# Kernel tuning notes

Hardware: AMD Instinct MI355X
Metric: run time of the kernel (lower is better)

Reference implementation:

```python
import jax, jax.numpy as jnp
import numpy as np

B, C = 32768, 1000

def setup_inputs() -> dict:
    key = jax.random.key(0)
    k1, k2 = jax.random.split(key)
    pred = jax.random.normal(k1, (B, C), dtype=jnp.float32)
    target = jax.random.randint(k2, (B,), 0, C, dtype=jnp.int64)
    return {"pred": pred, "target": target}

def reference(pred, target):
    b, c = pred.shape
    # histogram of labels: replaces the per-class Python loop
    class_freq = jnp.zeros((c,), dtype=pred.dtype).at[target].add(1.0)
    # exp(pred) * freq, then log-normalize over classes (balanced softmax)
    scaled = jnp.exp(pred) * class_freq  # [B, C]
    log_norm = jnp.log(jnp.sum(scaled, axis=1, keepdims=True))  # [B, 1]
    logits = jnp.log(scaled) - log_norm  # [B, C]
    # one-hot multiply + sum == gather logit at target class
    picked = jnp.take_along_axis(logits, target[:, None], axis=1)  # [B, 1]
    return -jnp.sum(picked) / b
```

## Files before the change

### kernel.cpp

```cpp
#include <hip/hip_runtime.h>

#define B_ROWS 32768
#define C_COLS 1000
#define NF4 250
#define MAIN_BLOCKS 2048
#define WAVES_TOTAL (MAIN_BLOCKS * 4)
#define HIST_BLOCKS 16
#define BINS_PER_BLOCK 64

__global__ __launch_bounds__(256) void bsl_hist(const int* __restrict__ target,
                                                float* __restrict__ freq) {
    __shared__ unsigned int lh[1024];
    const int tid = threadIdx.x;
    #pragma unroll
    for (int i = tid; i < 1024; i += 256) lh[i] = 0u;
    __syncthreads();
    const int4* t4 = reinterpret_cast<const int4*>(target);
    #pragma unroll 8
    for (int k = 0; k < 32; ++k) {
        int4 v = t4[tid + k * 256];
        atomicAdd(&lh[v.x], 1u);
        atomicAdd(&lh[v.y], 1u);
        atomicAdd(&lh[v.z], 1u);
        atomicAdd(&lh[v.w], 1u);
    }
    __syncthreads();
    if (tid < BINS_PER_BLOCK) {
        const int bin = blockIdx.x * BINS_PER_BLOCK + tid;
        freq[bin] = (float)lh[bin];
    }
}

__global__ __launch_bounds__(256) void bsl_main(const float* __restrict__ pred,
                                                const int* __restrict__ target,
                                                const float* __restrict__ freq,
                                                float* __restrict__ partials) {
    __shared__ float sfreq[C_COLS];
    __shared__ float swave[4];
    const int tid = threadIdx.x;
    const int lane = tid & 63;
    const int wib = tid >> 6;

    for (int i = tid; i < C_COLS; i += 256) sfreq[i] = freq[i];
    __syncthreads();
    const float4* sf4 = reinterpret_cast<const float4*>(sfreq);

    const int gwid = blockIdx.x * 4 + wib;
    float local = 0.0f;

    for (int row = gwid; row < B_ROWS; row += WAVES_TOTAL) {
        const int t = target[row];
        const float4* prow = reinterpret_cast<const float4*>(pred + (size_t)row * C_COLS);
        const int t4i = t >> 2, tm = t & 3;
        float partial = 0.0f, pt = 0.0f;
        #pragma unroll
        for (int k = 0; k < 4; ++k) {
            const int j = k * 64 + lane;
            if (j < NF4) {
                const float4 v = prow[j];
                const float4 f = sf4[j];
                partial += __expf(v.x) * f.x + __expf(v.y) * f.y
                         + __expf(v.z) * f.z + __expf(v.w) * f.w;
                if (j == t4i)
                    pt = (tm & 1) ? ((tm & 2) ? v.w : v.y)
                                  : ((tm & 2) ? v.z : v.x);
            }
        }
        #pragma unroll
        for (int off = 32; off > 0; off >>= 1)
            partial += __shfl_xor(partial, off, 64);
        const float ptb = __shfl(pt, t4i & 63, 64);
        local += logf(partial) - ptb - logf(sfreq[t]);
    }

    if (lane == 0) swave[wib] = local;
    __syncthreads();
    if (tid == 0)
        partials[blockIdx.x] = swave[0] + swave[1] + swave[2] + swave[3];
}

__global__ __launch_bounds__(256) void bsl_finalize(const float* __restrict__ partials,
                                                    float* __restrict__ out) {
    const int tid = threadIdx.x;
    float s = 0.0f;
    for (int i = tid; i < MAIN_BLOCKS; i += 256) s += partials[i];
    #pragma unroll
    for (int off = 32; off > 0; off >>= 1) s += __shfl_xor(s, off, 64);
    __shared__ float sw[4];
    if ((tid & 63) == 0) sw[tid >> 6] = s;
    __syncthreads();
    if (tid == 0) out[0] = (sw[0] + sw[1] + sw[2] + sw[3]) / (float)B_ROWS;
}

extern "C" void kernel_launch(void* const* d_in, const int* in_sizes, int n_in,
                              void* d_out, int out_size, void* d_ws, size_t ws_size,
                              hipStream_t stream) {
    const float* pred = (const float*)d_in[0];
    const int* target = (const int*)d_in[1];

    float* freq     = (float*)d_ws;
    float* partials = freq + 1024;

    bsl_hist<<<HIST_BLOCKS, 256, 0, stream>>>(target, freq);
    bsl_main<<<MAIN_BLOCKS, 256, 0, stream>>>(pred, target, freq, partials);
    bsl_finalize<<<1, 256, 0, stream>>>(partials, (float*)d_out);
}
```

Measured before the change: 38.57 us.

## Software-pipeline row loads with double-buffered registers in main kernel

Replaces the strided row loop with a fully unrolled four-row sequence per wave, preloading all target indices and double-buffering float4 row data in registers so the next row's global loads are in flight while the current row computes. It also adds a min-blocks-per-CU hint to launch bounds. The aim is to hide memory latency in a bandwidth-bound kernel, at the cost of more registers and a hardcoded assumption of exactly four rows per wave.

```diff
diff --git a/kernel.cpp b/kernel.cpp
--- a/kernel.cpp
+++ b/kernel.cpp
@@ -31,10 +31,10 @@
     }
 }
 
-__global__ __launch_bounds__(256) void bsl_main(const float* __restrict__ pred,
-                                                const int* __restrict__ target,
-                                                const float* __restrict__ freq,
-                                                float* __restrict__ partials) {
+__global__ __launch_bounds__(256, 8) void bsl_main(const float* __restrict__ pred,
+                                                   const int* __restrict__ target,
+                                                   const float* __restrict__ freq,
+                                                   float* __restrict__ partials) {
     __shared__ float sfreq[C_COLS];
     __shared__ float swave[4];
     const int tid = threadIdx.x;
@@ -46,32 +46,61 @@
     const float4* sf4 = reinterpret_cast<const float4*>(sfreq);
 
     const int gwid = blockIdx.x * 4 + wib;
+
+    const int t0 = target[gwid];
+    const int t1 = target[gwid + WAVES_TOTAL];
+    const int t2 = target[gwid + 2 * WAVES_TOTAL];
+    const int t3 = target[gwid + 3 * WAVES_TOTAL];
+
+    float4 va[4], vb[4];
     float local = 0.0f;
 
-    for (int row = gwid; row < B_ROWS; row += WAVES_TOTAL) {
-        const int t = target[row];
-        const float4* prow = reinterpret_cast<const float4*>(pred + (size_t)row * C_COLS);
-        const int t4i = t >> 2, tm = t & 3;
-        float partial = 0.0f, pt = 0.0f;
-        #pragma unroll
-        for (int k = 0; k < 4; ++k) {
-            const int j = k * 64 + lane;
-            if (j < NF4) {
-                const float4 v = prow[j];
-                const float4 f = sf4[j];
-                partial += __expf(v.x) * f.x + __expf(v.y) * f.y
-                         + __expf(v.z) * f.z + __expf(v.w) * f.w;
-                if (j == t4i)
-                    pt = (tm & 1) ? ((tm & 2) ? v.w : v.y)
-                                  : ((tm & 2) ? v.z : v.x);
-            }
-        }
-        #pragma unroll
-        for (int off = 32; off > 0; off >>= 1)
-            partial += __shfl_xor(partial, off, 64);
-        const float ptb = __shfl(pt, t4i & 63, 64);
-        local += logf(partial) - ptb - logf(sfreq[t]);
+#define LOADV(V, ROW)                                                          \
+    {                                                                          \
+        const float4* pp =                                                     \
+            reinterpret_cast<const float4*>(pred + (size_t)(ROW) * C_COLS);   \
+        _Pragma("unroll")                                                      \
+        for (int k = 0; k < 4; ++k) {                                          \
+            const int j = k * 64 + lane;                                       \
+            if (j < NF4) V[k] = pp[j];                                         \
+        }                                                                      \
     }
+
+#define COMPUTEV(V, T)                                                         \
+    {                                                                          \
+        const int t4i = (T) >> 2, tm = (T) & 3;                                \
+        float partial = 0.0f, pt = 0.0f;                                       \
+        _Pragma("unroll")                                                      \
+        for (int k = 0; k < 4; ++k) {                                          \
+            const int j = k * 64 + lane;                                       \
+            if (j < NF4) {                                                     \
+                const float4 f = sf4[j];                                       \
+                const float4 a = V[k];                                         \
+                partial += __expf(a.x) * f.x + __expf(a.y) * f.y               \
+                         + __expf(a.z) * f.z + __expf(a.w) * f.w;              \
+                if (j == t4i)                                                  \
+                    pt = (tm & 1) ? ((tm & 2) ? a.w : a.y)                     \
+                                  : ((tm & 2) ? a.z : a.x);                    \
+            }                                                                  \
+        }                                                                      \
+        _Pragma("unroll")                                                      \
+        for (int off = 32; off > 0; off >>= 1)                                 \
+            partial += __shfl_xor(partial, off, 64);                           \
+        const float ptb = __shfl(pt, t4i & 63, 64);                            \
+        local += logf(partial) - ptb - logf(sfreq[T]);                         \
+    }
+
+    LOADV(va, gwid);
+    LOADV(vb, gwid + WAVES_TOTAL);
+    COMPUTEV(va, t0);
+    LOADV(va, gwid + 2 * WAVES_TOTAL);
+    COMPUTEV(vb, t1);
+    LOADV(vb, gwid + 3 * WAVES_TOTAL);
+    COMPUTEV(va, t2);
+    COMPUTEV(vb, t3);
+
+#undef LOADV
+#undef COMPUTEV
 
     if (lane == 0) swave[wib] = local;
     __syncthreads();
```

Measured after the change: 42.05 us. +9.0%, slower.
